# Kernel tuning notes

Hardware: AMD Instinct MI355X
Metric: run time of the kernel (lower is better)

Reference implementation:

```python
import jax, jax.numpy as jnp
import numpy as np

B, N, C, H = 2, 256, 512, 8
D = C // H
SCALER = 1.0 / np.sqrt(D)


def setup_inputs() -> dict:
    key = jax.random.key(0)
    k1, k2 = jax.random.split(key)
    hidden_state = jax.random.normal(k1, (B, N, C), dtype=jnp.float32)
    # Linear(C -> 5C), no bias. Torch Linear stores W as [out, in]; y = x @ W.T
    W = jax.random.normal(k2, (5 * C, C), dtype=jnp.float32) * np.float32(1.0 / np.sqrt(C))
    return {"hidden_state": hidden_state, "W": W}


def reference(hidden_state, W):
    b_, n, c = hidden_state.shape
    w = hidden_state @ W.T                                   # [B,N,5C]
    w = w.reshape(b_, n, 5, H, D).transpose(2, 0, 3, 1, 4)   # [5,B,H,N,D]
    a, bq, cq, v1, v2 = w[0], w[1], w[2], w[3], w[4]

    # Pairwise score matrices with the (unscaled) clamped position bias min(j-i,0).
    # NOTE: the original code computes ALiBi slopes / position_bias_encoder but never
    # adds them to X/Y/Z -- only `position_bias` is added. We replicate that exactly.
    idx = jnp.arange(n)
    pb = jnp.minimum(idx[None, :] - idx[:, None], 0).astype(hidden_state.dtype)  # [N,N]

    X = jnp.einsum('bhid,bhjd->bhij', a, bq) * SCALER + pb   # [B,H,N,N]
    Y = jnp.einsum('bhjd,bhkd->bhjk', bq, cq) * SCALER + pb
    Z = jnp.einsum('bhkd,bhid->bhki', cq, a) * SCALER + pb

    # 3-way stabilized exponentials (axis choices match the torch code)
    X = jnp.exp(X - jnp.max(X, axis=-1, keepdims=True))
    Y = jnp.exp(Y - jnp.max(Y, axis=(-2, -1), keepdims=True))
    Z = jnp.exp(Z - jnp.max(Z, axis=-2, keepdims=True))

    # up_{id} = sum_{j,k} X_ij Y_jk Z_ki v1_jd v2_kd  (V = outer(v1, v2) is implicit)
    T = jnp.einsum('bhij,bhjk,bhjd->bhikd', X, Y, v1)        # [B,H,N,N,D]
    up = jnp.einsum('bhikd,bhki,bhkd->bhid', T, Z, v2)       # [B,H,N,D]

    down = jnp.einsum('bhij,bhjk,bhki->bhi', X, Y, Z) + 1e-9 # [B,H,N]
    att = up / down[..., None]
    return att.transpose(0, 2, 1, 3).reshape(b_, n, c)       # [B,N,C]
```

## Files before the change

### kernel.cpp

```cpp
#include <hip/hip_runtime.h>
#include <math.h>

#define NN 256
#define HH 8
#define DD 64
#define BH 16
#define SCALER 0.125f

#define REG     (BH*NN*DD)
#define MAT_SZ  (BH*NN*NN)
#define OFF_XH  0
#define OFF_V1T 524288
#define OFF_QKV 0
#define OFF_X   1310720
#define OFF_Y   (OFF_X + MAT_SZ)
#define OFF_Z   (OFF_Y + MAT_SZ)
#define OFF_MX  (OFF_Z + MAT_SZ)
#define OFF_MY  (OFF_MX + BH*NN)
#define OFF_MZ  (OFF_MY + 16)
#define OFF_YT  4464656
#define OFF_V2T 4988944
#define KB      4
#define OFF_UP  5251088
#define OFF_DN  6299664

typedef _Float16 f16x8 __attribute__((ext_vector_type(8)));
typedef _Float16 f16x4 __attribute__((ext_vector_type(4)));
typedef float    f32x4 __attribute__((ext_vector_type(4)));

__global__ __launch_bounds__(256) void k_proj(const float* __restrict__ Hs,
                                              const float* __restrict__ W,
                                              float* __restrict__ qkv) {
  __shared__ float As[16][68];
  __shared__ float Bs[16][68];
  const int bx = blockIdx.x, by = blockIdx.y;
  const int tid = threadIdx.x;
  const int ri = tid >> 4, ci = tid & 15;
  const int o0 = bx * 64, m0 = by * 64;
  float acc[4][4] = {};
  for (int k0 = 0; k0 < 512; k0 += 16) {
    __syncthreads();
    {
      const int m = tid >> 2, kq = (tid & 3) * 4;
      float4 va = *(const float4*)&Hs[(m0 + m) * 512 + k0 + kq];
      As[kq + 0][m] = va.x; As[kq + 1][m] = va.y; As[kq + 2][m] = va.z; As[kq + 3][m] = va.w;
      float4 vb = *(const float4*)&W[(o0 + m) * 512 + k0 + kq];
      Bs[kq + 0][m] = vb.x; Bs[kq + 1][m] = vb.y; Bs[kq + 2][m] = vb.z; Bs[kq + 3][m] = vb.w;
    }
    __syncthreads();
#pragma unroll
    for (int kk = 0; kk < 16; ++kk) {
      float4 a = *(const float4*)&As[kk][ri * 4];
      float4 b = *(const float4*)&Bs[kk][ci * 4];
      acc[0][0] += a.x * b.x; acc[0][1] += a.x * b.y; acc[0][2] += a.x * b.z; acc[0][3] += a.x * b.w;
      acc[1][0] += a.y * b.x; acc[1][1] += a.y * b.y; acc[1][2] += a.y * b.z; acc[1][3] += a.y * b.w;
      acc[2][0] += a.z * b.x; acc[2][1] += a.z * b.y; acc[2][2] += a.z * b.z; acc[2][3] += a.z * b.w;
      acc[3][0] += a.w * b.x; acc[3][1] += a.w * b.y; acc[3][2] += a.w * b.z; acc[3][3] += a.w * b.w;
    }
  }
  const int p = o0 >> 9;
  const int h = (o0 >> 6) & 7;
  const int d0 = ci * 4;
#pragma unroll
  for (int l = 0; l < 4; ++l) {
    const int r = m0 + ri * 4 + l;
    const int b = r >> 8, n = r & 255;
    float* dst = qkv + p * REG + (b * 8 + h) * (NN * DD) + n * DD + d0;
    *(float4*)dst = make_float4(acc[l][0], acc[l][1], acc[l][2], acc[l][3]);
  }
}

__global__ __launch_bounds__(256) void k_scores(const float* __restrict__ qkv,
                                                float* __restrict__ ws) {
  __shared__ float Us[32][68];
  __shared__ float Ws_[32][68];
  const int ms = blockIdx.z, bh = blockIdx.y;
  const int tr = blockIdx.x >> 3, tc = blockIdx.x & 7;
  const float* U; const float* Wm; float* O;
  if (ms == 0)      { U = qkv + 0 * REG; Wm = qkv + 1 * REG; O = ws + OFF_X; }
  else if (ms == 1) { U = qkv + 1 * REG; Wm = qkv + 2 * REG; O = ws + OFF_Y; }
  else              { U = qkv + 2 * REG; Wm = qkv + 0 * REG; O = ws + OFF_Z; }
  U  += bh * (NN * DD);
  Wm += bh * (NN * DD);
  O  += bh * (NN * NN);
  const int i0 = tr * 32, k0 = tc * 32;
  const int tid = threadIdx.x;
  {
    const int r = tid >> 3, d8 = (tid & 7) * 8;
    *(float4*)&Us[r][d8]      = *(const float4*)&U[(i0 + r) * DD + d8];
    *(float4*)&Us[r][d8 + 4]  = *(const float4*)&U[(i0 + r) * DD + d8 + 4];
    *(float4*)&Ws_[r][d8]     = *(const float4*)&Wm[(k0 + r) * DD + d8];
    *(float4*)&Ws_[r][d8 + 4] = *(const float4*)&Wm[(k0 + r) * DD + d8 + 4];
  }
  __syncthreads();
  const int ri = tid >> 4, ci = tid & 15;
  float a00 = 0.f, a01 = 0.f, a10 = 0.f, a11 = 0.f;
#pragma unroll
  for (int dd = 0; dd < 16; ++dd) {
    float4 u0 = *(const float4*)&Us[ri][dd * 4];
    float4 u1 = *(const float4*)&Us[ri + 16][dd * 4];
    float4 w0 = *(const float4*)&Ws_[ci][dd * 4];
    float4 w1 = *(const float4*)&Ws_[ci + 16][dd * 4];
    a00 += u0.x * w0.x + u0.y * w0.y + u0.z * w0.z + u0.w * w0.w;
    a01 += u0.x * w1.x + u0.y * w1.y + u0.z * w1.z + u0.w * w1.w;
    a10 += u1.x * w0.x + u1.y * w0.y + u1.z * w0.z + u1.w * w0.w;
    a11 += u1.x * w1.x + u1.y * w1.y + u1.z * w1.z + u1.w * w1.w;
  }
#define STORE_SC(accv, rr, cc) { \
    int row = (rr), col = (cc); \
    O[row * NN + col] = (accv) * SCALER + fminf((float)(col - row), 0.f); }
  STORE_SC(a00, i0 + ri,      k0 + ci)
  STORE_SC(a01, i0 + ri,      k0 + ci + 16)
  STORE_SC(a10, i0 + ri + 16, k0 + ci)
  STORE_SC(a11, i0 + ri + 16, k0 + ci + 16)
#undef STORE_SC
}

__global__ __launch_bounds__(256) void k_rowmax(const float* __restrict__ Xb, float* __restrict__ mx) {
  const int wid = threadIdx.x >> 6, lane = threadIdx.x & 63;
  const int gr = blockIdx.x * 4 + wid;
  float4 v = *(const float4*)&Xb[gr * 256 + lane * 4];
  float m = fmaxf(fmaxf(v.x, v.y), fmaxf(v.z, v.w));
#pragma unroll
  for (int off = 32; off; off >>= 1) m = fmaxf(m, __shfl_xor(m, off));
  if (lane == 0) mx[gr] = m;
}

__global__ __launch_bounds__(256) void k_gmax(const float* __restrict__ Yb, float* __restrict__ my) {
  const int bh = blockIdx.x, tid = threadIdx.x;
  const float4* p = (const float4*)(Yb + bh * (NN * NN));
  float m = -3.4e38f;
  for (int idx = tid; idx < 16384; idx += 256) {
    float4 v = p[idx];
    m = fmaxf(m, fmaxf(fmaxf(v.x, v.y), fmaxf(v.z, v.w)));
  }
#pragma unroll
  for (int off = 32; off; off >>= 1) m = fmaxf(m, __shfl_xor(m, off));
  __shared__ float red[4];
  if ((tid & 63) == 0) red[tid >> 6] = m;
  __syncthreads();
  if (tid == 0) my[bh] = fmaxf(fmaxf(red[0], red[1]), fmaxf(red[2], red[3]));
}

__global__ __launch_bounds__(256) void k_colmax(const float* __restrict__ Zb, float* __restrict__ mz) {
  const int bh = blockIdx.x, ic = blockIdx.y;
  const int il = threadIdx.x & 63, kp = threadIdx.x >> 6;
  const int i = ic * 64 + il;
  float m = -3.4e38f;
  for (int k = kp; k < 256; k += 4) m = fmaxf(m, Zb[bh * (NN * NN) + k * NN + i]);
  __shared__ float red[4][64];
  red[kp][il] = m;
  __syncthreads();
  if (kp == 0)
    mz[bh * NN + i] = fmaxf(fmaxf(red[0][il], red[1][il]), fmaxf(red[2][il], red[3][il]));
}

__global__ __launch_bounds__(256) void k_exp(float* __restrict__ ws) {
  const int g = blockIdx.x * 256 + threadIdx.x;
  const int buf = g / 262144, rem = g % 262144;
  const int bh = rem >> 14, rr = rem & 16383;
  const int row = rr >> 6, c4 = (rr & 63) * 4;
  float4* base = (float4*)(ws + (buf == 0 ? OFF_X : buf == 1 ? OFF_Y : OFF_Z));
  float4 v = base[rem];
  if (buf == 0) {
    float s = ws[OFF_MX + bh * NN + row];
    v.x = expf(v.x - s); v.y = expf(v.y - s); v.z = expf(v.z - s); v.w = expf(v.w - s);
  } else if (buf == 1) {
    float s = ws[OFF_MY + bh];
    v.x = expf(v.x - s); v.y = expf(v.y - s); v.z = expf(v.z - s); v.w = expf(v.w - s);
  } else {
    float4 s = *(const float4*)&ws[OFF_MZ + bh * NN + c4];
    v.x = expf(v.x - s.x); v.y = expf(v.y - s.y); v.z = expf(v.z - s.z); v.w = expf(v.w - s.w);
  }
  base[rem] = v;
}

__global__ __launch_bounds__(256) void k_cvt(float* __restrict__ ws) {
  __shared__ float T[64][65];
  const int blk = blockIdx.x, tid = threadIdx.x;
  if (blk < 256) {
    const float* X = ws + OFF_X;
    _Float16* Xh = (_Float16*)(ws + OFF_XH);
    const int base = (blk * 256 + tid) * 16;
#pragma unroll
    for (int q = 0; q < 4; ++q) {
      float4 v = *(const float4*)&X[base + q * 4];
      f16x4 o = {(_Float16)v.x, (_Float16)v.y, (_Float16)v.z, (_Float16)v.w};
      *(f16x4*)((_Float16*)&Xh[base + q * 4]) = o;
    }
  } else if (blk < 512) {
    const int b2 = blk - 256;
    const int bh = b2 >> 4, jt = (b2 >> 2) & 3, kt = b2 & 3;
    const float* Y = ws + OFF_Y + bh * 65536;
    _Float16* Yt = (_Float16*)(ws + OFF_YT) + bh * 65536;
    const int j0 = jt * 64, k0 = kt * 64;
#pragma unroll 4
    for (int p = 0; p < 16; ++p) {
      const int idx = p * 256 + tid, r = idx >> 6, c = idx & 63;
      T[r][c] = Y[(j0 + r) * 256 + k0 + c];
    }
    __syncthreads();
#pragma unroll 4
    for (int p = 0; p < 16; ++p) {
      const int idx = p * 256 + tid, r = idx >> 6, c = idx & 63;
      Yt[(k0 + r) * 256 + j0 + c] = (_Float16)T[c][r];
    }
  } else if (blk < 576) {
    const int b2 = blk - 512;
    const int bh = b2 >> 2, jt = b2 & 3;
    const float* v1 = ws + OFF_QKV + 3 * REG + bh * 16384;
    _Float16* v1t = (_Float16*)(ws + OFF_V1T) + bh * 16384;
    const int j0 = jt * 64;
#pragma unroll 4
    for (int p = 0; p < 16; ++p) {
      const int idx = p * 256 + tid, r = idx >> 6, c = idx & 63;
      T[r][c] = v1[(j0 + r) * 64 + c];
    }
    __syncthreads();
#pragma unroll 4
    for (int p = 0; p < 16; ++p) {
      const int idx = p * 256 + tid, r = idx >> 6, c = idx & 63;
      v1t[r * 256 + j0 + c] = (_Float16)T[c][r];
    }
  } else {
    const int b2 = blk - 576;
    const int bh = b2 >> 2, kt = b2 & 3;
    const float* v2 = ws + OFF_QKV + 4 * REG + bh * 16384;
    float* v2t = ws + OFF_V2T + bh * 16384;
    const int k0 = kt * 64;
#pragma unroll 4
    for (int p = 0; p < 16; ++p) {
      const int idx = p * 256 + tid, r = idx >> 6, c = idx & 63;
      T[r][c] = v2[(k0 + r) * 64 + c];
    }
    __syncthreads();
#pragma unroll 4
    for (int p = 0; p < 16; ++p) {
      const int idx = p * 256 + tid, r = idx >> 6, c = idx & 63;
      v2t[r * 256 + k0 + c] = T[c][r];
    }
  }
}

__global__ __launch_bounds__(512) void k_heavy(const float* __restrict__ ws,
                                               float* __restrict__ upP,
                                               float* __restrict__ dnP) {
  const int kb = blockIdx.x, ib = blockIdx.y, bh = blockIdx.z;
  const int k0 = kb * 64, i0 = ib * 64;
  const int tid = threadIdx.x;
  const int w = tid >> 6, lane = tid & 63;
  const int k16 = w & 3, ihalf = w >> 2;
  const int li = lane & 15, grp = lane >> 4;

  __shared__ _Float16 v1s[64 * 256];
  __shared__ float v2s[64 * 64];
  __shared__ float up_lds[64][68];
  __shared__ float dn_lds[64];

  const _Float16* Xh  = (const _Float16*)(ws + OFF_XH);
  const _Float16* Yt  = (const _Float16*)(ws + OFF_YT);
  const _Float16* v1t = (const _Float16*)(ws + OFF_V1T);
  const float*    v2t = ws + OFF_V2T;
  const float*    Zp  = ws + OFF_Z + bh * 65536;

  {
    const float4* src = (const float4*)(v1t + bh * 16384);
    float4* dst = (float4*)v1s;
    for (int t = tid; t < 2048; t += 512) dst[t] = src[t];
  }
  {
    const int d = tid >> 3, kq = (tid & 7) * 8;
    const float* s = v2t + bh * 16384 + d * 256 + k0 + kq;
    *(float4*)&v2s[d * 64 + kq]     = *(const float4*)s;
    *(float4*)&v2s[d * 64 + kq + 4] = *(const float4*)(s + 4);
  }
  for (int t = tid; t < 64 * 68; t += 512) ((float*)up_lds)[t] = 0.f;
  if (tid < 64) dn_lds[tid] = 0.f;

  f16x8 Yf[8];
  {
    const _Float16* yb = Yt + (long)bh * 65536 + (k0 + k16 * 16 + li) * 256 + grp * 8;
#pragma unroll
    for (int js = 0; js < 8; ++js) Yf[js] = *(const f16x8*)(yb + js * 32);
  }
  f16x8 Xf0[8], Xf1[8];
  {
    const _Float16* xb0 = Xh + (long)bh * 65536 + (i0 + (ihalf * 2 + 0) * 16 + li) * 256 + grp * 8;
    const _Float16* xb1 = Xh + (long)bh * 65536 + (i0 + (ihalf * 2 + 1) * 16 + li) * 256 + grp * 8;
#pragma unroll
    for (int js = 0; js < 8; ++js) { Xf0[js] = *(const f16x8*)(xb0 + js * 32); Xf1[js] = *(const f16x8*)(xb1 + js * 32); }
  }
  float Zr0[4], Zr1[4];
#pragma unroll
  for (int r = 0; r < 4; ++r) {
    const int kk = (k0 + k16 * 16 + grp * 4 + r) * 256 + i0;
    Zr0[r] = Zp[kk + (ihalf * 2 + 0) * 16 + li];
    Zr1[r] = Zp[kk + (ihalf * 2 + 1) * 16 + li];
  }

  __syncthreads();

  const int ir0 = (ihalf * 2 + 0) * 16 + li;
  const int ir1 = (ihalf * 2 + 1) * 16 + li;

  for (int it = 0; it < 64; ++it) {
    f32x4 acc0 = {0.f, 0.f, 0.f, 0.f}, acc1 = {0.f, 0.f, 0.f, 0.f};
#pragma unroll
    for (int js = 0; js < 8; ++js) {
      f16x8 vf = *(const f16x8*)&v1s[it * 256 + js * 32 + grp * 8];
      f16x8 ad = Yf[js] * vf;
      acc0 = __builtin_amdgcn_mfma_f32_16x16x32_f16(ad, Xf0[js], acc0, 0, 0, 0);
      acc1 = __builtin_amdgcn_mfma_f32_16x16x32_f16(ad, Xf1[js], acc1, 0, 0, 0);
    }
    f32x4 w2 = *(const f32x4*)&v2s[it * 64 + k16 * 16 + grp * 4];
    float s0 = (acc0[0] * Zr0[0]) * w2[0] + (acc0[1] * Zr0[1]) * w2[1]
             + (acc0[2] * Zr0[2]) * w2[2] + (acc0[3] * Zr0[3]) * w2[3];
    float s1 = (acc1[0] * Zr1[0]) * w2[0] + (acc1[1] * Zr1[1]) * w2[1]
             + (acc1[2] * Zr1[2]) * w2[2] + (acc1[3] * Zr1[3]) * w2[3];
    s0 += __shfl_xor(s0, 16); s0 += __shfl_xor(s0, 32);
    s1 += __shfl_xor(s1, 16); s1 += __shfl_xor(s1, 32);
    if (lane < 16) {
      atomicAdd(&up_lds[ir0][it], s0);
      atomicAdd(&up_lds[ir1][it], s1);
    }
  }
  {
    f32x4 acc0 = {0.f, 0.f, 0.f, 0.f}, acc1 = {0.f, 0.f, 0.f, 0.f};
#pragma unroll
    for (int js = 0; js < 8; ++js) {
      acc0 = __builtin_amdgcn_mfma_f32_16x16x32_f16(Yf[js], Xf0[js], acc0, 0, 0, 0);
      acc1 = __builtin_amdgcn_mfma_f32_16x16x32_f16(Yf[js], Xf1[js], acc1, 0, 0, 0);
    }
    float s0 = acc0[0] * Zr0[0] + acc0[1] * Zr0[1] + acc0[2] * Zr0[2] + acc0[3] * Zr0[3];
    float s1 = acc1[0] * Zr1[0] + acc1[1] * Zr1[1] + acc1[2] * Zr1[2] + acc1[3] * Zr1[3];
    s0 += __shfl_xor(s0, 16); s0 += __shfl_xor(s0, 32);
    s1 += __shfl_xor(s1, 16); s1 += __shfl_xor(s1, 32);
    if (lane < 16) {
      atomicAdd(&dn_lds[ir0], s0);
      atomicAdd(&dn_lds[ir1], s1);
    }
  }
  __syncthreads();
  {
    const int il = tid >> 3, dq = (tid & 7) * 8;
    float* dst = upP + ((long)((kb * 16 + bh) * 256) + i0 + il) * 64 + dq;
    *(float4*)dst       = *(const float4*)&up_lds[il][dq];
    *(float4*)(dst + 4) = *(const float4*)&up_lds[il][dq + 4];
  }
  if (tid < 64) dnP[(kb * 16 + bh) * 256 + i0 + tid] = dn_lds[tid];
}

__global__ __launch_bounds__(256) void k_final(const float* __restrict__ ws_in, float* __restrict__ out) {
  const int g = blockIdx.x * 256 + threadIdx.x;
  const int e0 = g * 4;
  const int c = e0 & 511, n = (e0 >> 9) & 255, b = e0 >> 17;
  const int h = c >> 6, d = c & 63;
  const int bh = b * 8 + h;
  const float* upP = ws_in + OFF_UP;
  const float* dnP = ws_in + OFF_DN;
  float4 acc = make_float4(0.f, 0.f, 0.f, 0.f);
  float dn = 0.f;
#pragma unroll
  for (int ks = 0; ks < KB; ++ks) {
    const float4 u = *(const float4*)&upP[((ks * 16 + bh) * 256 + n) * 64 + d];
    acc.x += u.x; acc.y += u.y; acc.z += u.z; acc.w += u.w;
    dn += dnP[(ks * 16 + bh) * 256 + n];
  }
  const float inv = 1.f / (dn + 1e-9f);
  acc.x *= inv; acc.y *= inv; acc.z *= inv; acc.w *= inv;
  *(float4*)&out[e0] = acc;
}

extern "C" void kernel_launch(void* const* d_in, const int* in_sizes, int n_in,
                              void* d_out, int out_size, void* d_ws, size_t ws_size,
                              hipStream_t stream) {
  (void)in_sizes; (void)n_in; (void)out_size; (void)ws_size;
  const float* hidden = (const float*)d_in[0];
  const float* W      = (const float*)d_in[1];
  float* ws  = (float*)d_ws;
  float* out = (float*)d_out;

  k_proj<<<dim3(40, 8), 256, 0, stream>>>(hidden, W, ws + OFF_QKV);
  k_scores<<<dim3(64, BH, 3), 256, 0, stream>>>(ws + OFF_QKV, ws);
  k_rowmax<<<dim3(1024), 256, 0, stream>>>(ws + OFF_X, ws + OFF_MX);
  k_gmax<<<dim3(16), 256, 0, stream>>>(ws + OFF_Y, ws + OFF_MY);
  k_colmax<<<dim3(16, 4), 256, 0, stream>>>(ws + OFF_Z, ws + OFF_MZ);
  k_exp<<<dim3(3072), 256, 0, stream>>>(ws);
  k_cvt<<<dim3(640), 256, 0, stream>>>(ws);
  k_heavy<<<dim3(KB, 4, BH), 512, 0, stream>>>(ws, ws + OFF_UP, ws + OFF_DN);
  k_final<<<dim3(256), 256, 0, stream>>>(ws, out);
}
```

Baseline: 203.0 us.

## Fuse max reductions and exp into conversion, split heavy kernel over D

Merges the row, global and column max kernels into one launch, and computes the Y global max in two stages through per-row maxima. Exponentiation is folded into the f16 conversion and transpose for X and Y, with only Z keeping an in-place fp32 exp pass. The heavy kernel now also splits the D dimension into four blocks, giving four times as many blocks with a smaller LDS footprint. LDS atomics are replaced by per-wave partial buffers that are summed at the end, and only one D-slice computes the denominator. The intent is fewer launches, less memory traffic and better occupancy, at the cost of recomputing the shared Y·X MFMA work in each D slice.

```diff
diff --git a/kernel.cpp b/kernel.cpp
--- a/kernel.cpp
+++ b/kernel.cpp
@@ -23,6 +23,7 @@
 #define KB      4
 #define OFF_UP  5251088
 #define OFF_DN  6299664
+#define OFF_YR  6316048
 
 typedef _Float16 f16x8 __attribute__((ext_vector_type(8)));
 typedef _Float16 f16x4 __attribute__((ext_vector_type(4)));
@@ -116,24 +117,40 @@
 #undef STORE_SC
 }
 
-__global__ __launch_bounds__(256) void k_rowmax(const float* __restrict__ Xb, float* __restrict__ mx) {
-  const int wid = threadIdx.x >> 6, lane = threadIdx.x & 63;
-  const int gr = blockIdx.x * 4 + wid;
-  float4 v = *(const float4*)&Xb[gr * 256 + lane * 4];
-  float m = fmaxf(fmaxf(v.x, v.y), fmaxf(v.z, v.w));
-#pragma unroll
-  for (int off = 32; off; off >>= 1) m = fmaxf(m, __shfl_xor(m, off));
-  if (lane == 0) mx[gr] = m;
-}
-
-__global__ __launch_bounds__(256) void k_gmax(const float* __restrict__ Yb, float* __restrict__ my) {
+__global__ __launch_bounds__(256) void k_maxes(const float* __restrict__ ws,
+                                               float* __restrict__ mx,
+                                               float* __restrict__ yrow,
+                                               float* __restrict__ mz) {
+  const int blk = blockIdx.x, tid = threadIdx.x;
+  if (blk < 2048) {
+    const int wid = tid >> 6, lane = tid & 63;
+    const float* base = ws + (blk < 1024 ? OFF_X : OFF_Y);
+    float* out = (blk < 1024) ? mx : yrow;
+    const int gr = (blk & 1023) * 4 + wid;
+    float4 v = *(const float4*)&base[gr * 256 + lane * 4];
+    float m = fmaxf(fmaxf(v.x, v.y), fmaxf(v.z, v.w));
+#pragma unroll
+    for (int off = 32; off; off >>= 1) m = fmaxf(m, __shfl_xor(m, off));
+    if (lane == 0) out[gr] = m;
+  } else {
+    const int b2 = blk - 2048;
+    const int bh = b2 >> 2, ic = b2 & 3;
+    const int il = tid & 63, kp = tid >> 6;
+    const int i = ic * 64 + il;
+    const float* Zb = ws + OFF_Z;
+    float m = -3.4e38f;
+    for (int k = kp; k < 256; k += 4) m = fmaxf(m, Zb[bh * (NN * NN) + k * NN + i]);
+    __shared__ float red[4][64];
+    red[kp][il] = m;
+    __syncthreads();
+    if (kp == 0)
+      mz[bh * NN + i] = fmaxf(fmaxf(red[0][il], red[1][il]), fmaxf(red[2][il], red[3][il]));
+  }
+}
+
+__global__ __launch_bounds__(256) void k_ymax2(const float* __restrict__ yrow, float* __restrict__ my) {
   const int bh = blockIdx.x, tid = threadIdx.x;
-  const float4* p = (const float4*)(Yb + bh * (NN * NN));
-  float m = -3.4e38f;
-  for (int idx = tid; idx < 16384; idx += 256) {
-    float4 v = p[idx];
-    m = fmaxf(m, fmaxf(fmaxf(v.x, v.y), fmaxf(v.z, v.w)));
-  }
+  float m = yrow[bh * 256 + tid];
 #pragma unroll
   for (int off = 32; off; off >>= 1) m = fmaxf(m, __shfl_xor(m, off));
   __shared__ float red[4];
@@ -142,57 +159,28 @@
   if (tid == 0) my[bh] = fmaxf(fmaxf(red[0], red[1]), fmaxf(red[2], red[3]));
 }
 
-__global__ __launch_bounds__(256) void k_colmax(const float* __restrict__ Zb, float* __restrict__ mz) {
-  const int bh = blockIdx.x, ic = blockIdx.y;
-  const int il = threadIdx.x & 63, kp = threadIdx.x >> 6;
-  const int i = ic * 64 + il;
-  float m = -3.4e38f;
-  for (int k = kp; k < 256; k += 4) m = fmaxf(m, Zb[bh * (NN * NN) + k * NN + i]);
-  __shared__ float red[4][64];
-  red[kp][il] = m;
-  __syncthreads();
-  if (kp == 0)
-    mz[bh * NN + i] = fmaxf(fmaxf(red[0][il], red[1][il]), fmaxf(red[2][il], red[3][il]));
-}
-
-__global__ __launch_bounds__(256) void k_exp(float* __restrict__ ws) {
-  const int g = blockIdx.x * 256 + threadIdx.x;
-  const int buf = g / 262144, rem = g % 262144;
-  const int bh = rem >> 14, rr = rem & 16383;
-  const int row = rr >> 6, c4 = (rr & 63) * 4;
-  float4* base = (float4*)(ws + (buf == 0 ? OFF_X : buf == 1 ? OFF_Y : OFF_Z));
-  float4 v = base[rem];
-  if (buf == 0) {
-    float s = ws[OFF_MX + bh * NN + row];
-    v.x = expf(v.x - s); v.y = expf(v.y - s); v.z = expf(v.z - s); v.w = expf(v.w - s);
-  } else if (buf == 1) {
-    float s = ws[OFF_MY + bh];
-    v.x = expf(v.x - s); v.y = expf(v.y - s); v.z = expf(v.z - s); v.w = expf(v.w - s);
-  } else {
-    float4 s = *(const float4*)&ws[OFF_MZ + bh * NN + c4];
-    v.x = expf(v.x - s.x); v.y = expf(v.y - s.y); v.z = expf(v.z - s.z); v.w = expf(v.w - s.w);
-  }
-  base[rem] = v;
-}
-
-__global__ __launch_bounds__(256) void k_cvt(float* __restrict__ ws) {
+__global__ __launch_bounds__(256) void k_cvtexp(float* __restrict__ ws) {
   __shared__ float T[64][65];
   const int blk = blockIdx.x, tid = threadIdx.x;
   if (blk < 256) {
     const float* X = ws + OFF_X;
     _Float16* Xh = (_Float16*)(ws + OFF_XH);
-    const int base = (blk * 256 + tid) * 16;
+    const int gt = blk * 256 + tid;
+    const int base = gt * 16;
+    const float s = ws[OFF_MX + (gt >> 4)];
 #pragma unroll
     for (int q = 0; q < 4; ++q) {
       float4 v = *(const float4*)&X[base + q * 4];
-      f16x4 o = {(_Float16)v.x, (_Float16)v.y, (_Float16)v.z, (_Float16)v.w};
-      *(f16x4*)((_Float16*)&Xh[base + q * 4]) = o;
+      f16x4 o = {(_Float16)expf(v.x - s), (_Float16)expf(v.y - s),
+                 (_Float16)expf(v.z - s), (_Float16)expf(v.w - s)};
+      *(f16x4*)&Xh[base + q * 4] = o;
     }
   } else if (blk < 512) {
     const int b2 = blk - 256;
     const int bh = b2 >> 4, jt = (b2 >> 2) & 3, kt = b2 & 3;
     const float* Y = ws + OFF_Y + bh * 65536;
     _Float16* Yt = (_Float16*)(ws + OFF_YT) + bh * 65536;
+    const float s = ws[OFF_MY + bh];
     const int j0 = jt * 64, k0 = kt * 64;
 #pragma unroll 4
     for (int p = 0; p < 16; ++p) {
@@ -203,7 +191,7 @@
 #pragma unroll 4
     for (int p = 0; p < 16; ++p) {
       const int idx = p * 256 + tid, r = idx >> 6, c = idx & 63;
-      Yt[(k0 + r) * 256 + j0 + c] = (_Float16)T[c][r];
+      Yt[(k0 + r) * 256 + j0 + c] = (_Float16)expf(T[c][r] - s);
     }
   } else if (blk < 576) {
     const int b2 = blk - 512;
@@ -222,7 +210,7 @@
       const int idx = p * 256 + tid, r = idx >> 6, c = idx & 63;
       v1t[r * 256 + j0 + c] = (_Float16)T[c][r];
     }
-  } else {
+  } else if (blk < 640) {
     const int b2 = blk - 576;
     const int bh = b2 >> 2, kt = b2 & 3;
     const float* v2 = ws + OFF_QKV + 4 * REG + bh * 16384;
@@ -239,23 +227,33 @@
       const int idx = p * 256 + tid, r = idx >> 6, c = idx & 63;
       v2t[r * 256 + k0 + c] = T[c][r];
     }
+  } else {
+    const int rem = (blk - 640) * 256 + tid;
+    const int bh = rem >> 14, rr = rem & 16383;
+    const int c4 = (rr & 63) * 4;
+    float4* base = (float4*)(ws + OFF_Z);
+    float4 v = base[rem];
+    float4 s = *(const float4*)&ws[OFF_MZ + bh * NN + c4];
+    v.x = expf(v.x - s.x); v.y = expf(v.y - s.y); v.z = expf(v.z - s.z); v.w = expf(v.w - s.w);
+    base[rem] = v;
   }
 }
 
 __global__ __launch_bounds__(512) void k_heavy(const float* __restrict__ ws,
                                                float* __restrict__ upP,
                                                float* __restrict__ dnP) {
-  const int kb = blockIdx.x, ib = blockIdx.y, bh = blockIdx.z;
-  const int k0 = kb * 64, i0 = ib * 64;
+  const int kb = blockIdx.x, ib = blockIdx.y, zz = blockIdx.z;
+  const int bh = zz >> 2, dp = zz & 3;
+  const int k0 = kb * 64, i0 = ib * 64, d0 = dp * 16;
   const int tid = threadIdx.x;
   const int w = tid >> 6, lane = tid & 63;
   const int k16 = w & 3, ihalf = w >> 2;
   const int li = lane & 15, grp = lane >> 4;
 
-  __shared__ _Float16 v1s[64 * 256];
-  __shared__ float v2s[64 * 64];
-  __shared__ float up_lds[64][68];
-  __shared__ float dn_lds[64];
+  __shared__ _Float16 v1s[16 * 256];
+  __shared__ float v2s[16 * 64];
+  __shared__ float up_l[4][64][20];
+  __shared__ float dn_l[4][64];
 
   const _Float16* Xh  = (const _Float16*)(ws + OFF_XH);
   const _Float16* Yt  = (const _Float16*)(ws + OFF_YT);
@@ -264,18 +262,13 @@
   const float*    Zp  = ws + OFF_Z + bh * 65536;
 
   {
-    const float4* src = (const float4*)(v1t + bh * 16384);
-    float4* dst = (float4*)v1s;
-    for (int t = tid; t < 2048; t += 512) dst[t] = src[t];
-  }
-  {
-    const int d = tid >> 3, kq = (tid & 7) * 8;
-    const float* s = v2t + bh * 16384 + d * 256 + k0 + kq;
-    *(float4*)&v2s[d * 64 + kq]     = *(const float4*)s;
-    *(float4*)&v2s[d * 64 + kq + 4] = *(const float4*)(s + 4);
-  }
-  for (int t = tid; t < 64 * 68; t += 512) ((float*)up_lds)[t] = 0.f;
-  if (tid < 64) dn_lds[tid] = 0.f;
+    const float4* src = (const float4*)(v1t + bh * 16384 + d0 * 256);
+    ((float4*)v1s)[tid] = src[tid];
+  }
+  if (tid < 256) {
+    const int d = tid >> 4, kq = (tid & 15) * 4;
+    *(float4*)&v2s[d * 64 + kq] = *(const float4*)&v2t[bh * 16384 + (d0 + d) * 256 + k0 + kq];
+  }
 
   f16x8 Yf[8];
   {
@@ -303,7 +296,7 @@
   const int ir0 = (ihalf * 2 + 0) * 16 + li;
   const int ir1 = (ihalf * 2 + 1) * 16 + li;
 
-  for (int it = 0; it < 64; ++it) {
+  for (int it = 0; it < 16; ++it) {
     f32x4 acc0 = {0.f, 0.f, 0.f, 0.f}, acc1 = {0.f, 0.f, 0.f, 0.f};
 #pragma unroll
     for (int js = 0; js < 8; ++js) {
@@ -320,11 +313,11 @@
     s0 += __shfl_xor(s0, 16); s0 += __shfl_xor(s0, 32);
     s1 += __shfl_xor(s1, 16); s1 += __shfl_xor(s1, 32);
     if (lane < 16) {
-      atomicAdd(&up_lds[ir0][it], s0);
-      atomicAdd(&up_lds[ir1][it], s1);
-    }
-  }
-  {
+      up_l[k16][ir0][it] = s0;
+      up_l[k16][ir1][it] = s1;
+    }
+  }
+  if (dp == 3) {
     f32x4 acc0 = {0.f, 0.f, 0.f, 0.f}, acc1 = {0.f, 0.f, 0.f, 0.f};
 #pragma unroll
     for (int js = 0; js < 8; ++js) {
@@ -336,18 +329,21 @@
     s0 += __shfl_xor(s0, 16); s0 += __shfl_xor(s0, 32);
     s1 += __shfl_xor(s1, 16); s1 += __shfl_xor(s1, 32);
     if (lane < 16) {
-      atomicAdd(&dn_lds[ir0], s0);
-      atomicAdd(&dn_lds[ir1], s1);
+      dn_l[k16][ir0] = s0;
+      dn_l[k16][ir1] = s1;
     }
   }
   __syncthreads();
   {
-    const int il = tid >> 3, dq = (tid & 7) * 8;
-    float* dst = upP + ((long)((kb * 16 + bh) * 256) + i0 + il) * 64 + dq;
-    *(float4*)dst       = *(const float4*)&up_lds[il][dq];
-    *(float4*)(dst + 4) = *(const float4*)&up_lds[il][dq + 4];
-  }
-  if (tid < 64) dnP[(kb * 16 + bh) * 256 + i0 + tid] = dn_lds[tid];
+    const int il = tid >> 3, dq = (tid & 7) * 2;
+    float a = up_l[0][il][dq]     + up_l[1][il][dq]     + up_l[2][il][dq]     + up_l[3][il][dq];
+    float b = up_l[0][il][dq + 1] + up_l[1][il][dq + 1] + up_l[2][il][dq + 1] + up_l[3][il][dq + 1];
+    float* dst = upP + ((long)((kb * 16 + bh) * 256) + i0 + il) * 64 + d0 + dq;
+    dst[0] = a; dst[1] = b;
+  }
+  if (dp == 3 && tid < 64)
+    dnP[(kb * 16 + bh) * 256 + i0 + tid] =
+        dn_l[0][tid] + dn_l[1][tid] + dn_l[2][tid] + dn_l[3][tid];
 }
 
 __global__ __launch_bounds__(256) void k_final(const float* __restrict__ ws_in, float* __restrict__ out) {
@@ -382,11 +378,9 @@
 
   k_proj<<<dim3(40, 8), 256, 0, stream>>>(hidden, W, ws + OFF_QKV);
   k_scores<<<dim3(64, BH, 3), 256, 0, stream>>>(ws + OFF_QKV, ws);
-  k_rowmax<<<dim3(1024), 256, 0, stream>>>(ws + OFF_X, ws + OFF_MX);
-  k_gmax<<<dim3(16), 256, 0, stream>>>(ws + OFF_Y, ws + OFF_MY);
-  k_colmax<<<dim3(16, 4), 256, 0, stream>>>(ws + OFF_Z, ws + OFF_MZ);
-  k_exp<<<dim3(3072), 256, 0, stream>>>(ws);
-  k_cvt<<<dim3(640), 256, 0, stream>>>(ws);
-  k_heavy<<<dim3(KB, 4, BH), 512, 0, stream>>>(ws, ws + OFF_UP, ws + OFF_DN);
+  k_maxes<<<dim3(2112), 256, 0, stream>>>(ws, ws + OFF_MX, ws + OFF_YR, ws + OFF_MZ);
+  k_ymax2<<<dim3(16), 256, 0, stream>>>(ws + OFF_YR, ws + OFF_MY);
+  k_cvtexp<<<dim3(1664), 256, 0, stream>>>(ws);
+  k_heavy<<<dim3(KB, 4, 64), 512, 0, stream>>>(ws, ws + OFF_UP, ws + OFF_DN);
   k_final<<<dim3(256), 256, 0, stream>>>(ws, out);
 }
```

After: 191.4 us. -5.7%, faster.
